# Kernel optimization log

Hardware: AMD Instinct MI355X
Metric: run time of the kernel (lower is better)

The kernel has to match this reference:

```python
import jax, jax.numpy as jnp
import numpy as np

SOM_NODES = 1024
Z_DIM = 256
SOM_1D = int(np.sqrt(SOM_NODES))  # 32
N_EPOCHS = 100
SIGMA_END = 0.5
SIGMA_0 = np.sqrt(SOM_NODES) // 2  # 16.0
_DECAY = -N_EPOCHS / np.log(SIGMA_END / SIGMA_0)
SIGMAS = SIGMA_0 * np.exp(-np.arange(N_EPOCHS) / _DECAY)  # epoch -> sigma
BS = 65536


def setup_inputs() -> dict:
    key = jax.random.key(0)
    k1, k2 = jax.random.split(key)
    z_e = jax.random.normal(k1, (BS, Z_DIM), dtype=jnp.float32)
    # embedding init: uniform(-sqrt(1/z_dim), sqrt(1/z_dim))
    lim = np.sqrt(1.0 / Z_DIM)
    codebook = jax.random.uniform(k2, (SOM_NODES, Z_DIM), dtype=jnp.float32,
                                  minval=-lim, maxval=lim)
    return {"z_e": z_e, "codebook": codebook, "epoch": 50}


def _pairwise_sq_dists(x, y):
    # ||x_i - y_j||^2, clamped at 0
    x_norm = jnp.sum(x * x, axis=1, keepdims=True)          # [bs, 1]
    y_norm = jnp.sum(y * y, axis=1)[None, :]                # [1, N]
    dist = x_norm + y_norm - 2.0 * (x @ y.T)                # [bs, N]
    return jnp.maximum(dist, 0.0)


def _neighbour_weighing(k, epoch):
    # k: [bs] int32/int64 selected node indices
    k_x = k // SOM_1D
    k_y = k % SOM_1D
    xx, yy = jnp.meshgrid(jnp.arange(SOM_1D), jnp.arange(SOM_1D), indexing="ij")
    xxf = xx.reshape(-1).astype(jnp.float32)                # [N]
    yyf = yy.reshape(-1).astype(jnp.float32)
    dx = xxf[None, :] - k_y[:, None].astype(jnp.float32)    # [bs, N]
    dy = yyf[None, :] - k_x[:, None].astype(jnp.float32)
    dist_grid = dx * dx + dy * dy                           # squared euclidean
    sigma = SIGMAS[epoch]
    w = jnp.exp(-dist_grid / (2.0 * sigma * sigma))
    return w.reshape(-1, SOM_1D, SOM_1D)


def reference(z_e, codebook, epoch):
    distance_matrix = _pairwise_sq_dists(z_e, codebook)     # [bs, N]
    k = jnp.argmin(distance_matrix, axis=-1)                # [bs]
    # one-hot codebook selection (equivalent to gather, keeps codebook grad path)
    z_q = codebook[k]                                       # [bs, z_dim]
    neighbour_weighing = _neighbour_weighing(k, epoch)      # [bs, 32, 32]
    return z_e, k, z_q, neighbour_weighing, distance_matrix
```

## Files before the change

kernel.cpp:

```cpp
#include <hip/hip_runtime.h>
#include <hip/hip_bf16.h>
#include <math.h>

#define BATCH 65536
#define NODES 1024
#define ZD    256
#define KSA   512
#define KSB   768
#define EPSGAP 1.5e-3f
#define RB    8

#define OFF_ZE   0ull
#define OFF_K    16777216ull
#define OFF_ZQ   16842752ull
#define OFF_NW   33619968ull
#define OFF_DIST 100728832ull

typedef __attribute__((ext_vector_type(8))) short short8v;
typedef __attribute__((ext_vector_type(4))) float f32x4;

#define GLOAD16(g, l) __builtin_amdgcn_global_load_lds( \
    (const __attribute__((address_space(1))) void*)(g), \
    (__attribute__((address_space(3))) void*)(l), 16, 0, 0)

__device__ inline float wave_reduce_add(float s) {
#pragma unroll
    for (int off = 32; off; off >>= 1) s += __shfl_down(s, off);
    return s;
}

__device__ inline void nt_store4(float* p, float4 v) {
    f32x4 t = {v.x, v.y, v.z, v.w};
    __builtin_nontemporal_store(t, (f32x4*)p);
}

__global__ __launch_bounds__(256) void split_k(const float* __restrict__ X,
                                               ushort* __restrict__ P,
                                               float* __restrict__ norms,
                                               float* __restrict__ copy_out,
                                               int* __restrict__ zero_cnt,
                                               int isA) {
    if (zero_cnt && blockIdx.x == 0 && threadIdx.x == 0) *zero_cnt = 0;
    int row  = blockIdx.x * 4 + (threadIdx.x >> 6);
    int lane = threadIdx.x & 63;
    float4 v = ((const float4*)(X + (size_t)row * ZD))[lane];
    if (copy_out) nt_store4(copy_out + (size_t)row * ZD + lane * 4, v);
    float s = v.x * v.x + v.y * v.y + v.z * v.z + v.w * v.w;
    s = wave_reduce_add(s);
    if (lane == 0) norms[row] = s;

    float xs[4] = {v.x, v.y, v.z, v.w};
    ushort hi[4], lo[4];
#pragma unroll
    for (int i = 0; i < 4; ++i) {
        __hip_bfloat16 h = __float2bfloat16(xs[i]);
        float hf = __bfloat162float(h);
        __hip_bfloat16 l = __float2bfloat16(xs[i] - hf);
        hi[i] = *(ushort*)&h;
        lo[i] = *(ushort*)&l;
    }
    ushort4 h4 = make_ushort4(hi[0], hi[1], hi[2], hi[3]);
    ushort4 l4 = make_ushort4(lo[0], lo[1], lo[2], lo[3]);
    if (isA) {
        ushort* base = P + (size_t)row * KSA + lane * 4;
        *(ushort4*)(base)       = h4;
        *(ushort4*)(base + 256) = l4;
    } else {
        ushort* base = P + (size_t)row * KSB + lane * 4;
        *(ushort4*)(base)       = h4;
        *(ushort4*)(base + 256) = l4;
        *(ushort4*)(base + 512) = h4;
    }
}

__global__ __launch_bounds__(256, 4) void dist_mfma_k(const ushort* __restrict__ Ap,
                                                      const ushort* __restrict__ Bp,
                                                      const float* __restrict__ xn,
                                                      const float* __restrict__ yn,
                                                      float* __restrict__ D,
                                                      float4* __restrict__ partials) {
    __shared__ ushort As[128 * 64];
    __shared__ ushort Bs[128 * 64];

    const int tid  = threadIdx.x;
    const int lane = tid & 63;
    const int wave = tid >> 6;
    const int wr = wave >> 1, wc = wave & 1;

    int orig = blockIdx.x;
    int wg = (orig & 7) * 512 + (orig >> 3);
    const int bm = wg >> 3, bn = wg & 7;

    f32x4 acc[4][4];
#pragma unroll
    for (int i = 0; i < 4; ++i)
#pragma unroll
        for (int j = 0; j < 4; ++j) acc[i][j] = f32x4{0.f, 0.f, 0.f, 0.f};

    const int sg    = tid & 7;
    const int srow0 = tid >> 3;

    auto stage = [&](int kstep) {
        int a_koff = ((kstep < 4) ? kstep : (kstep - 4)) * 64;
#pragma unroll
        for (int i = 0; i < 4; ++i) {
            int row = i * 32 + srow0;
            int ss = sg ^ (row & 7);
            const ushort* ga = Ap + (size_t)(bm * 128 + row) * KSA + a_koff + ss * 8;
            GLOAD16(ga, &As[(row * 8 + sg) * 8]);
            const ushort* gb = Bp + (size_t)(bn * 128 + row) * KSB + kstep * 64 + ss * 8;
            GLOAD16(gb, &Bs[(row * 8 + sg) * 8]);
        }
    };

    const int frow = lane & 15;
    const int fk   = lane >> 4;
    int a_off[4], a_x7[4], b_off[4], b_x7[4];
#pragma unroll
    for (int f = 0; f < 4; ++f) {
        int ar = wr * 64 + f * 16 + frow;
        a_off[f] = ar * 64;  a_x7[f] = ar & 7;
        int br = wc * 64 + f * 16 + frow;
        b_off[f] = br * 64;  b_x7[f] = br & 7;
    }

    auto compute = [&]() {
#pragma unroll
        for (int k32 = 0; k32 < 2; ++k32) {
            int skb = k32 * 4 + fk;
            short8v af[4], bf[4];
#pragma unroll
            for (int f = 0; f < 4; ++f)
                af[f] = *(const short8v*)&As[a_off[f] + ((skb ^ a_x7[f]) * 8)];
#pragma unroll
            for (int f = 0; f < 4; ++f)
                bf[f] = *(const short8v*)&Bs[b_off[f] + ((skb ^ b_x7[f]) * 8)];
#pragma unroll
            for (int i = 0; i < 4; ++i)
#pragma unroll
                for (int j = 0; j < 4; ++j)
                    acc[i][j] = __builtin_amdgcn_mfma_f32_16x16x32_bf16(bf[i], af[j], acc[i][j], 0, 0, 0);
        }
    };

    for (int ks = 0; ks < 12; ++ks) {
        stage(ks);
        __syncthreads();
        compute();
        __syncthreads();
    }

    const int n0 = bn * 128 + wc * 64 + fk * 4;
    float4 ynv[4];
#pragma unroll
    for (int fn = 0; fn < 4; ++fn) ynv[fn] = *(const float4*)(yn + n0 + fn * 16);

    float4* red = (float4*)&As[0];

#pragma unroll
    for (int fm = 0; fm < 4; ++fm) {
        const int mloc = wr * 64 + fm * 16 + frow;
        const size_t M = (size_t)(bm * 128 + mloc);
        float xv = xn[M];
        float* drow = D + M * NODES;
        float v1 = 3.4e38f, v2 = 3.4e38f;
        int   c1 = 1 << 30,  c2 = 1 << 30;
#pragma unroll
        for (int fn = 0; fn < 4; ++fn) {
            f32x4 a = acc[fn][fm];
            float4 d;
            d.x = fmaxf(xv + ynv[fn].x - 2.0f * a[0], 0.0f);
            d.y = fmaxf(xv + ynv[fn].y - 2.0f * a[1], 0.0f);
            d.z = fmaxf(xv + ynv[fn].z - 2.0f * a[2], 0.0f);
            d.w = fmaxf(xv + ynv[fn].w - 2.0f * a[3], 0.0f);
            nt_store4(drow + n0 + fn * 16, d);
            float dv[4] = {d.x, d.y, d.z, d.w};
#pragma unroll
            for (int j = 0; j < 4; ++j) {
                int c = n0 + fn * 16 + j;
                if (dv[j] < v1 || (dv[j] == v1 && c < c1)) { v2 = v1; c2 = c1; v1 = dv[j]; c1 = c; }
                else if (dv[j] < v2 || (dv[j] == v2 && c < c2)) { v2 = dv[j]; c2 = c; }
            }
        }
#pragma unroll
        for (int off = 16; off < 64; off <<= 1) {
            float w1 = __shfl_xor(v1, off); int d1 = __shfl_xor(c1, off);
            float w2 = __shfl_xor(v2, off); int d2 = __shfl_xor(c2, off);
            if (w1 < v1 || (w1 == v1 && d1 < c1)) { v2 = v1; c2 = c1; v1 = w1; c1 = d1; }
            else if (w1 < v2 || (w1 == v2 && d1 < c2)) { v2 = w1; c2 = d1; }
            if (w2 < v2 || (w2 == v2 && d2 < c2)) {
                if (w2 < v1 || (w2 == v1 && d2 < c1)) { v2 = v1; c2 = c1; v1 = w2; c1 = d2; }
                else { v2 = w2; c2 = d2; }
            }
        }
        if (fk == 0) red[mloc * 2 + wc] = make_float4(v1, (float)c1, v2, (float)c2);
    }
    __syncthreads();
    if (tid < 128) {
        float4 a = red[tid * 2 + 0];
        float4 b = red[tid * 2 + 1];
        float v1 = a.x, c1 = a.y, v2 = a.z, c2 = a.w;
        if (b.x < v1 || (b.x == v1 && b.y < c1)) { v2 = v1; c2 = c1; v1 = b.x; c1 = b.y; }
        else if (b.x < v2 || (b.x == v2 && b.y < c2)) { v2 = b.x; c2 = b.y; }
        if (b.z < v2 || (b.z == v2 && b.w < c2)) {
            if (b.z < v1 || (b.z == v1 && b.w < c1)) { v2 = v1; c2 = c1; v1 = b.z; c1 = b.w; }
            else { v2 = b.z; c2 = b.w; }
        }
        partials[(size_t)(bm * 128 + tid) * 8 + bn] = make_float4(v1, c1, v2, c2);
    }
}

__global__ __launch_bounds__(256) void finish1_k(const float4* __restrict__ partials,
                                                 float* __restrict__ out_k,
                                                 int* __restrict__ refine_cnt,
                                                 int* __restrict__ refine_list) {
    int r = blockIdx.x * 256 + threadIdx.x;
    float v1 = 3.4e38f, c1 = 2.0e9f, v2 = 3.4e38f, c2 = 2.0e9f;
#pragma unroll
    for (int i = 0; i < 8; ++i) {
        float4 p = partials[(size_t)r * 8 + i];
        if (p.x < v1 || (p.x == v1 && p.y < c1)) { v2 = v1; c2 = c1; v1 = p.x; c1 = p.y; }
        else if (p.x < v2 || (p.x == v2 && p.y < c2)) { v2 = p.x; c2 = p.y; }
        if (p.z < v2 || (p.z == v2 && p.w < c2)) {
            if (p.z < v1 || (p.z == v1 && p.w < c1)) { v2 = v1; c2 = c1; v1 = p.z; c1 = p.w; }
            else { v2 = p.z; c2 = p.w; }
        }
    }
    out_k[r] = c1;
    if (v2 - v1 < EPSGAP) {
        int slot = atomicAdd(refine_cnt, 1);
        refine_list[slot] = r;
    }
}

__global__ __launch_bounds__(256) void refine_k(const float* __restrict__ ze,
                                                const float* __restrict__ cb,
                                                const float* __restrict__ xn,
                                                const float* __restrict__ yn,
                                                const int* __restrict__ refine_cnt,
                                                const int* __restrict__ refine_list,
                                                float* __restrict__ out_k) {
    __shared__ float zs[RB][ZD];
    __shared__ float rvs[RB][4];
    __shared__ int   rcs[RB][4];
    const int n   = *refine_cnt;
    const int tid = threadIdx.x;
    const int lane = tid & 63, w = tid >> 6;

    for (int base = blockIdx.x * RB; base < n; base += gridDim.x * RB) {
        int nb = n - base; if (nb > RB) nb = RB;
        __syncthreads();
        {
            int rr = tid >> 5, p = tid & 31;
            if (rr < nb) {
                int r = refine_list[base + rr];
                const float4* zp = (const float4*)(ze + (size_t)r * ZD);
                ((float4*)zs[rr])[p]      = zp[p];
                ((float4*)zs[rr])[p + 32] = zp[p + 32];
            }
        }
        __syncthreads();

        float dot[RB][4];
#pragma unroll
        for (int rr = 0; rr < RB; ++rr)
#pragma unroll
            for (int m = 0; m < 4; ++m) dot[rr][m] = 0.0f;

        for (int k4 = 0; k4 < 64; ++k4) {
            float4 c[4];
#pragma unroll
            for (int m = 0; m < 4; ++m)
                c[m] = *(const float4*)(cb + (size_t)(tid + m * 256) * ZD + k4 * 4);
#pragma unroll
            for (int rr = 0; rr < RB; ++rr) {
                float4 zv = ((const float4*)zs[rr])[k4];
#pragma unroll
                for (int m = 0; m < 4; ++m) {
                    float d = dot[rr][m];
                    d = fmaf(zv.x, c[m].x, d);
                    d = fmaf(zv.y, c[m].y, d);
                    d = fmaf(zv.z, c[m].z, d);
                    d = fmaf(zv.w, c[m].w, d);
                    dot[rr][m] = d;
                }
            }
        }

        float ynv[4];
#pragma unroll
        for (int m = 0; m < 4; ++m) ynv[m] = yn[tid + m * 256];

        for (int rr = 0; rr < nb; ++rr) {
            int r = refine_list[base + rr];
            float xv = xn[r];
            float bv = 3.4e38f; int bc = 1 << 30;
#pragma unroll
            for (int m = 0; m < 4; ++m) {
                int j = tid + m * 256;
                float d = fmaxf((xv + ynv[m]) - 2.0f * dot[rr][m], 0.0f);
                if (d < bv) { bv = d; bc = j; }
            }
#pragma unroll
            for (int off = 32; off; off >>= 1) {
                float ov = __shfl_down(bv, off);
                int   oc = __shfl_down(bc, off);
                if (ov < bv || (ov == bv && oc < bc)) { bv = ov; bc = oc; }
            }
            if (lane == 0) { rvs[rr][w] = bv; rcs[rr][w] = bc; }
        }
        __syncthreads();
        if (tid < nb) {
            float fv = rvs[tid][0]; int fc = rcs[tid][0];
#pragma unroll
            for (int i = 1; i < 4; ++i)
                if (rvs[tid][i] < fv || (rvs[tid][i] == fv && rcs[tid][i] < fc)) { fv = rvs[tid][i]; fc = rcs[tid][i]; }
            out_k[refine_list[base + tid]] = (float)fc;
        }
    }
}

__global__ __launch_bounds__(256) void finish2_k(const float* __restrict__ cb,
                                                 const int* __restrict__ epoch_p,
                                                 const float* __restrict__ kf,
                                                 float* __restrict__ out_zq,
                                                 float* __restrict__ out_nw) {
    __shared__ float g[32];

    int ep = epoch_p[0];
    double sig = 16.0 * exp((double)ep * -0.034657359027997265);
    float ninv = (float)(-1.0 / (2.0 * sig * sig));
    if (threadIdx.x < 32) {
        float t = (float)threadIdx.x;
        g[threadIdx.x] = __expf(t * t * ninv);
    }
    __syncthreads();

    int row  = blockIdx.x * 4 + (threadIdx.x >> 6);
    int lane = threadIdx.x & 63;
    int k = (int)kf[row];

    nt_store4(out_zq + (size_t)row * ZD + lane * 4,
              ((const float4*)(cb + (size_t)k * ZD))[lane]);

    int kx = k >> 5, ky = k & 31;
    float* nwp = out_nw + (size_t)row * NODES;
#pragma unroll
    for (int i = 0; i < 4; ++i) {
        int q = i * 64 + lane;
        int n = q * 4;
        int nx = n >> 5;
        int ny = n & 31;
        float gx = g[abs(nx - ky)];
        float4 w;
        w.x = gx * g[abs(ny + 0 - kx)];
        w.y = gx * g[abs(ny + 1 - kx)];
        w.z = gx * g[abs(ny + 2 - kx)];
        w.w = gx * g[abs(ny + 3 - kx)];
        nt_store4(nwp + q * 4, w);
    }
}

extern "C" void kernel_launch(void* const* d_in, const int* in_sizes, int n_in,
                              void* d_out, int out_size, void* d_ws, size_t ws_size,
                              hipStream_t stream) {
    const float* z_e      = (const float*)d_in[0];
    const float* codebook = (const float*)d_in[1];
    const int*   epoch_p  = (const int*)d_in[2];
    float* out = (float*)d_out;

    char* scratch = (char*)(out + OFF_NW);
    ushort* Ap = (ushort*)scratch;
    ushort* Bp = (ushort*)(scratch + 67108864);
    float*  xn = (float*) (scratch + 68681728);
    float*  yn = (float*) (scratch + 68943872);
    float4* partials = (float4*)(scratch + 68947968);
    int* refine_cnt  = (int*)(out + OFF_ZQ);
    int* refine_list = refine_cnt + 1;

    split_k<<<BATCH / 4, 256, 0, stream>>>(z_e, Ap, xn, out + OFF_ZE, nullptr, 1);
    split_k<<<NODES / 4, 256, 0, stream>>>(codebook, Bp, yn, nullptr, refine_cnt, 0);

    dist_mfma_k<<<4096, 256, 0, stream>>>(Ap, Bp, xn, yn, out + OFF_DIST, partials);

    finish1_k<<<BATCH / 256, 256, 0, stream>>>(partials, out + OFF_K, refine_cnt, refine_list);
    refine_k<<<512, 256, 0, stream>>>(z_e, codebook, xn, yn, refine_cnt, refine_list, out + OFF_K);
    finish2_k<<<BATCH / 4, 256, 0, stream>>>(codebook, epoch_p, out + OFF_K,
                                             out + OFF_ZQ, out + OFF_NW);
}
```

Measured before the change: 270.4 us.

## Double-buffer LDS tiles in distance GEMM to overlap loads with MFMA

Doubles the shared-memory A/B tiles and prefetches the next k-step via global_load_lds while the current tile is consumed by MFMA. Explicit vmcnt waits and raw s_barrier replace the two __syncthreads per step, and launch bounds drop to 2 blocks per CU to fit the doubled LDS. This is meant to hide global load latency in the GEMM main loop, at the cost of lower occupancy and a larger LDS footprint.

```diff
diff --git a/kernel.cpp b/kernel.cpp
--- a/kernel.cpp
+++ b/kernel.cpp
@@ -73,14 +73,14 @@
     }
 }
 
-__global__ __launch_bounds__(256, 4) void dist_mfma_k(const ushort* __restrict__ Ap,
+__global__ __launch_bounds__(256, 2) void dist_mfma_k(const ushort* __restrict__ Ap,
                                                       const ushort* __restrict__ Bp,
                                                       const float* __restrict__ xn,
                                                       const float* __restrict__ yn,
                                                       float* __restrict__ D,
                                                       float4* __restrict__ partials) {
-    __shared__ ushort As[128 * 64];
-    __shared__ ushort Bs[128 * 64];
+    __shared__ ushort As[2][128 * 64];
+    __shared__ ushort Bs[2][128 * 64];
 
     const int tid  = threadIdx.x;
     const int lane = tid & 63;
@@ -100,16 +100,16 @@
     const int sg    = tid & 7;
     const int srow0 = tid >> 3;
 
-    auto stage = [&](int kstep) {
+    auto stage = [&](int buf, int kstep) {
         int a_koff = ((kstep < 4) ? kstep : (kstep - 4)) * 64;
 #pragma unroll
         for (int i = 0; i < 4; ++i) {
             int row = i * 32 + srow0;
             int ss = sg ^ (row & 7);
             const ushort* ga = Ap + (size_t)(bm * 128 + row) * KSA + a_koff + ss * 8;
-            GLOAD16(ga, &As[(row * 8 + sg) * 8]);
+            GLOAD16(ga, &As[buf][(row * 8 + sg) * 8]);
             const ushort* gb = Bp + (size_t)(bn * 128 + row) * KSB + kstep * 64 + ss * 8;
-            GLOAD16(gb, &Bs[(row * 8 + sg) * 8]);
+            GLOAD16(gb, &Bs[buf][(row * 8 + sg) * 8]);
         }
     };
 
@@ -124,17 +124,17 @@
         b_off[f] = br * 64;  b_x7[f] = br & 7;
     }
 
-    auto compute = [&]() {
+    auto compute = [&](int buf) {
 #pragma unroll
         for (int k32 = 0; k32 < 2; ++k32) {
             int skb = k32 * 4 + fk;
             short8v af[4], bf[4];
 #pragma unroll
             for (int f = 0; f < 4; ++f)
-                af[f] = *(const short8v*)&As[a_off[f] + ((skb ^ a_x7[f]) * 8)];
+                af[f] = *(const short8v*)&As[buf][a_off[f] + ((skb ^ a_x7[f]) * 8)];
 #pragma unroll
             for (int f = 0; f < 4; ++f)
-                bf[f] = *(const short8v*)&Bs[b_off[f] + ((skb ^ b_x7[f]) * 8)];
+                bf[f] = *(const short8v*)&Bs[buf][b_off[f] + ((skb ^ b_x7[f]) * 8)];
 #pragma unroll
             for (int i = 0; i < 4; ++i)
 #pragma unroll
@@ -143,11 +143,18 @@
         }
     };
 
+    stage(0, 0);
+#pragma unroll
     for (int ks = 0; ks < 12; ++ks) {
-        stage(ks);
-        __syncthreads();
-        compute();
-        __syncthreads();
+        int cur = ks & 1;
+        if (ks < 11) stage(cur ^ 1, ks + 1);
+        if (ks < 11) asm volatile("s_waitcnt vmcnt(8)" ::: "memory");
+        else         asm volatile("s_waitcnt vmcnt(0)" ::: "memory");
+        __builtin_amdgcn_s_barrier();
+        __builtin_amdgcn_sched_barrier(0);
+        compute(cur);
+        asm volatile("s_waitcnt lgkmcnt(0)" ::: "memory");
+        __builtin_amdgcn_s_barrier();
     }
 
     const int n0 = bn * 128 + wc * 64 + fk * 4;
@@ -155,7 +162,7 @@
 #pragma unroll
     for (int fn = 0; fn < 4; ++fn) ynv[fn] = *(const float4*)(yn + n0 + fn * 16);
 
-    float4* red = (float4*)&As[0];
+    float4* red = (float4*)&As[0][0];
 
 #pragma unroll
     for (int fm = 0; fm < 4; ++fm) {
```

Result: slower. 292.0 us (+8.0%).
